# Kernel optimization log

Measured on AMD Instinct MI355X. Metric: run time of the kernel, lower is better.

The kernel has to match this reference:

```python
import jax, jax.numpy as jnp
import numpy as np

B, S, H, E = 32, 4096, 512, 512

def setup_inputs() -> dict:
    key = jax.random.key(0)
    ks = jax.random.split(key, 11)
    sc = 1.0 / np.sqrt(H)
    return {
        "context": jax.random.normal(ks[0], (B, S, H), jnp.float32),
        "h": jax.random.normal(ks[1], (B, H), jnp.float32),
        "x": jax.random.normal(ks[2], (B, E), jnp.float32),
        "We": jax.random.normal(ks[3], (H, H), jnp.float32) * sc,
        "be": jax.random.normal(ks[4], (H,), jnp.float32) * sc,
        "Wd": jax.random.normal(ks[5], (H, H), jnp.float32) * sc,
        "bd": jax.random.normal(ks[6], (H,), jnp.float32) * sc,
        "Wv": jax.random.normal(ks[7], (H,), jnp.float32) * sc,
        "bv": jax.random.normal(ks[8], (1,), jnp.float32) * sc,
        "Wr": jax.random.normal(ks[9], (2 * H, 2 * H + E), jnp.float32) * (1.0 / np.sqrt(2 * H + E)),
        "br": jax.random.normal(ks[10], (2 * H,), jnp.float32) * sc,
    }

def reference(context, h, x, We, be, Wd, bd, Wv, bv, Wr, br):
    # gamma_encoder: [B,S,H]; gamma_decoder: [B,1,H]
    ge = jnp.einsum('bsh,kh->bsk', context, We) + be
    gd = h @ Wd.T + bd
    # additive scores -> [B,S]
    scores = jnp.einsum('bsh,h->bs', jnp.tanh(ge + gd[:, None, :]), Wv) + bv[0]
    weights = jax.nn.softmax(scores, axis=1)
    # context vector c_t: [B,H]
    c_t = jnp.einsum('bs,bsh->bh', weights, context)
    # linear_r on [c_t, h, x] -> [B,2H]
    r_t = jnp.concatenate([c_t, h, x], axis=1) @ Wr.T + br
    # maxout over pairs: view [B,H,2].max(-1)
    output = jnp.max(r_t.reshape(-1, r_t.shape[1] // 2, 2), axis=2)
    return (output, weights)
```

## Files before the change

### kernel.cpp

```cpp
#include <hip/hip_runtime.h>

typedef __attribute__((ext_vector_type(8))) short bf16x8;
typedef __attribute__((ext_vector_type(16))) float f32x16;

typedef __attribute__((address_space(3))) unsigned int lds_u32;
typedef __attribute__((address_space(1))) unsigned int glb_u32;

union frag_u { bf16x8 v; unsigned int u[4]; };

__device__ inline unsigned int cvt_pk_bf16(float lo, float hi){
  unsigned int r;
  asm("v_cvt_pk_bf16_f32 %0, %1, %2" : "=v"(r) : "v"(lo), "v"(hi));
  return r;
}
__device__ inline bf16x8 pack8(float4 a, float4 b){
  union { unsigned int u[4]; bf16x8 v; } r;
  r.u[0]=cvt_pk_bf16(a.x,a.y); r.u[1]=cvt_pk_bf16(a.z,a.w);
  r.u[2]=cvt_pk_bf16(b.x,b.y); r.u[3]=cvt_pk_bf16(b.z,b.w);
  return r.v;
}
__device__ inline float fast_tanh(float x){
  float e = __builtin_amdgcn_exp2f(x * 2.8853900817779268f);
  return 1.0f - 2.0f * __builtin_amdgcn_rcpf(e + 1.0f);
}
#define PIN8(F) asm volatile("" : "+v"((F).u[0]), "+v"((F).u[1]), \
                                  "+v"((F).u[2]), "+v"((F).u[3]))
#define LOG2E 1.4426950408889634f

__global__ __launch_bounds__(256) void we_conv(const float* __restrict__ We,
                                               uint4* __restrict__ weFrag){
  int gid = blockIdx.x * 256 + threadIdx.x;
  int l  = gid & 63;
  int nc = gid >> 11;
  int t  = (gid >> 6) & 31;
  int colv = nc*32 + (l & 31);
  int k = t*16 + (l >> 5)*8;
  const float4* src = (const float4*)(We + colv*512 + k);
  float4 f0 = src[0], f1 = src[1];
  weFrag[gid] = make_uint4(cvt_pk_bf16(f0.x,f0.y), cvt_pk_bf16(f0.z,f0.w),
                           cvt_pk_bf16(f1.x,f1.y), cvt_pk_bf16(f1.z,f1.w));
}

__global__ __launch_bounds__(256) void gd_kernel(const float* __restrict__ hvec,
                                                 const float* __restrict__ Wd,
                                                 const float* __restrict__ bd,
                                                 const float* __restrict__ be,
                                                 float* __restrict__ gd){
  __shared__ float hs[512];
  int b = blockIdx.x >> 2, kc = blockIdx.x & 3;
  int tid = threadIdx.x;
  hs[tid]       = hvec[b*512 + tid];
  hs[tid + 256] = hvec[b*512 + 256 + tid];
  __syncthreads();
  int k  = kc*128 + (tid >> 1);
  int hh = (tid & 1) * 256;
  const float4* wrow = (const float4*)(Wd + (size_t)k*512 + hh);
  const float4* hv4  = (const float4*)(hs + hh);
  float acc = 0.f;
  #pragma unroll 8
  for (int i = 0; i < 64; ++i){
    float4 w = wrow[i]; float4 u = hv4[i];
    acc += w.x*u.x + w.y*u.y + w.z*u.z + w.w*u.w;
  }
  acc += __shfl_xor(acc, 1);
  if ((tid & 1) == 0) gd[b*512 + k] = acc + bd[k] + be[k];
}

__global__ __launch_bounds__(256, 2) void score_kernel(
    const float* __restrict__ ctx, const uint4* __restrict__ weFrag,
    const float* __restrict__ gd, const float* __restrict__ Wv,
    float* __restrict__ scores, float* __restrict__ ctp,
    float* __restrict__ MS){
  __shared__ char lds[2*32768 + 4096];
  __shared__ float sc_lds[128];
  __shared__ float w_lds[128];
  __shared__ float red2[2];
  char* ldsB = lds;
  float* gdwv = (float*)(lds + 65536);

  const int tid  = threadIdx.x;
  const int wid  = tid >> 6;
  const int lane = tid & 63;
  const int bid  = blockIdx.x;
  const int row0 = bid * 128;
  const int b    = bid >> 5;
  const int col  = lane & 31;
  const int hi   = lane >> 5;
  const int st   = bid & 15;

  #define ISSUE(NC, BUF) do { \
    const char* _g = (const char*)weFrag + (size_t)(NC)*32768 + wid*8192 + lane*16; \
    char* _l = ldsB + (BUF)*32768 + wid*8192; \
    _Pragma("unroll") \
    for (int _i = 0; _i < 8; ++_i) \
      __builtin_amdgcn_global_load_lds((const glb_u32*)(_g + _i*1024), \
                                       (lds_u32*)(_l + _i*1024), 16, 0, 0); \
  } while(0)

  ISSUE(st, 0);

  if (tid < 128) ((float4*)gdwv)[tid] = ((const float4*)(gd + b*512))[tid];
  else           ((float4*)gdwv)[tid] = ((const float4*)Wv)[tid - 128];

  frag_u afrag[32];
  {
    const float4* ap = (const float4*)(ctx + (size_t)(row0 + wid*32 + col)*512 + hi*8);
    #pragma unroll
    for (int t = 0; t < 32; ++t){
      afrag[t].v = pack8(ap[t*4], ap[t*4 + 1]);
      PIN8(afrag[t]);
    }
  }

  asm volatile("s_waitcnt lgkmcnt(0)" ::: "memory");

  float sc[16];
  #pragma unroll
  for (int r = 0; r < 16; ++r) sc[r] = 0.f;

  for (int nc = 0; nc < 16; ++nc){
    const int cur = (st + nc) & 15;
    asm volatile("s_waitcnt vmcnt(0)" ::: "memory");
    __builtin_amdgcn_s_barrier();
    if (nc < 15) ISSUE((cur + 1) & 15, (nc + 1) & 1);

    const char* bb = ldsB + (nc & 1)*32768 + lane*16;
    f32x16 accLo, accHi;
    #pragma unroll
    for (int r = 0; r < 16; ++r){ accLo[r] = 0.f; accHi[r] = 0.f; }

    frag_u c0, c1, c2, c3, n0, n1, n2, n3;
    c0.v = *(const bf16x8*)(bb +  0*1024);
    c1.v = *(const bf16x8*)(bb +  8*1024);
    c2.v = *(const bf16x8*)(bb + 16*1024);
    c3.v = *(const bf16x8*)(bb + 24*1024);
    PIN8(c0); PIN8(c1); PIN8(c2); PIN8(c3);

    #pragma unroll
    for (int g = 0; g < 8; ++g){
      if (g < 7){
        n0.v = *(const bf16x8*)(bb + (g + 1     )*1024);
        n1.v = *(const bf16x8*)(bb + (g + 1 +  8)*1024);
        n2.v = *(const bf16x8*)(bb + (g + 1 + 16)*1024);
        n3.v = *(const bf16x8*)(bb + (g + 1 + 24)*1024);
      }
      __builtin_amdgcn_s_setprio(1);
      accLo = __builtin_amdgcn_mfma_f32_32x32x16_bf16(afrag[g     ].v, c0.v, accLo, 0, 0, 0);
      accHi = __builtin_amdgcn_mfma_f32_32x32x16_bf16(afrag[g + 16].v, c2.v, accHi, 0, 0, 0);
      accLo = __builtin_amdgcn_mfma_f32_32x32x16_bf16(afrag[g +  8].v, c1.v, accLo, 0, 0, 0);
      accHi = __builtin_amdgcn_mfma_f32_32x32x16_bf16(afrag[g + 24].v, c3.v, accHi, 0, 0, 0);
      __builtin_amdgcn_s_setprio(0);
      if (g < 7){
        PIN8(n0); PIN8(n1); PIN8(n2); PIN8(n3);
        c0 = n0; c1 = n1; c2 = n2; c3 = n3;
      }
    }

    float gdv = gdwv[cur*32 + col];
    float wvv = gdwv[512 + cur*32 + col];
    #pragma unroll
    for (int r = 0; r < 16; ++r)
      sc[r] += fast_tanh(accLo[r] + accHi[r] + gdv) * wvv;
  }
  #undef ISSUE

  #pragma unroll
  for (int r = 0; r < 16; ++r){
    #pragma unroll
    for (int m = 1; m <= 16; m <<= 1) sc[r] += __shfl_xor(sc[r], m);
  }
  if (col == 0){
    float* so = scores + row0 + wid*32 + 4*hi;
    #pragma unroll
    for (int r = 0; r < 16; ++r){
      int rr = (r & 3) + 8*(r >> 2);
      so[rr] = sc[r];
      sc_lds[wid*32 + 4*hi + rr] = sc[r];
    }
  }
  __syncthreads();

  float M = -1e30f;
  {
    const float4* s4 = (const float4*)sc_lds;
    #pragma unroll
    for (int i = 0; i < 32; ++i){
      float4 v = s4[i];
      M = fmaxf(M, fmaxf(fmaxf(v.x, v.y), fmaxf(v.z, v.w)));
    }
  }
  if (tid < 128){
    float w = __builtin_amdgcn_exp2f((sc_lds[tid] - M) * LOG2E);
    w_lds[tid] = w;
    #pragma unroll
    for (int o = 1; o < 64; o <<= 1) w += __shfl_xor(w, o);
    if ((tid & 63) == 0) red2[tid >> 6] = w;
  }
  __syncthreads();
  float S_blk = red2[0] + red2[1];

  float ctpA = 0.f, ctpB = 0.f;
  #pragma unroll
  for (int p = 0; p < 2; ++p){
    if ((wid >> 1) == p){
      int rl = (wid & 1)*32 + col;
      char* dst = ldsB + rl*1024;
      int swz = (rl & 7) << 4;
      #pragma unroll
      for (int t = 0; t < 32; ++t)
        *(uint4*)(dst + ((t*32 + hi*16) ^ swz)) = *(uint4*)&afrag[t].u[0];
    }
    __syncthreads();
    const float* wp = w_lds + p*64;
    #pragma unroll 8
    for (int r = 0; r < 64; ++r){
      unsigned int u = *(const unsigned int*)(ldsB + r*1024 + ((tid*4) ^ ((r & 7) << 4)));
      float cw = wp[r];
      union { unsigned int q; float f; } flo, fhi;
      flo.q = u << 16;
      fhi.q = u & 0xffff0000u;
      ctpA += cw * flo.f;
      ctpB += cw * fhi.f;
    }
    __syncthreads();
  }
  ((float2*)(ctp + (size_t)bid*512))[tid] = make_float2(ctpA, ctpB);
  if (tid == 0){ MS[2*bid] = M; MS[2*bid + 1] = S_blk; }
}

__global__ __launch_bounds__(256) void combine_kernel(const float* __restrict__ ctp,
                                                      const float* __restrict__ MS,
                                                      float* __restrict__ ct,
                                                      float* __restrict__ mbuf){
  __shared__ float wsh[32];
  __shared__ float msh[2];
  int b = blockIdx.x, tid = threadIdx.x;
  if (tid < 64){
    int i = tid & 31;
    float Mi = MS[(b*32 + i)*2];
    float Si = MS[(b*32 + i)*2 + 1];
    float M = Mi;
    #pragma unroll
    for (int o = 1; o < 32; o <<= 1) M = fmaxf(M, __shfl_xor(M, o));
    float w = __builtin_amdgcn_exp2f((Mi - M) * LOG2E);
    float d = w * Si;
    #pragma unroll
    for (int o = 1; o < 32; o <<= 1) d += __shfl_xor(d, o);
    if (tid < 32) wsh[i] = w;
    if (tid == 0){ msh[0] = M; msh[1] = 1.0f / d; }
  }
  __syncthreads();
  float invd = msh[1];
  float a0 = 0.f, a1 = 0.f;
  #pragma unroll
  for (int i = 0; i < 32; ++i){
    float2 v = ((const float2*)(ctp + (size_t)(b*32 + i)*512))[tid];
    float w = wsh[i];
    a0 += w * v.x; a1 += w * v.y;
  }
  ((float2*)(ct + b*512))[tid] = make_float2(a0 * invd, a1 * invd);
  if (tid == 0){ mbuf[2*b] = msh[0]; mbuf[2*b + 1] = invd; }
}

__global__ __launch_bounds__(256) void weights_kernel(const float* __restrict__ scores,
                                                      const float* __restrict__ mbuf,
                                                      float* __restrict__ weights){
  int b = blockIdx.x, tid = threadIdx.x;
  float M = mbuf[2*b], invd = mbuf[2*b + 1];
  const float4* src = (const float4*)(scores + b*4096);
  float4* dst = (float4*)(weights + b*4096);
  #pragma unroll
  for (int i = 0; i < 4; ++i){
    float4 v = src[tid + i*256];
    v.x = __builtin_amdgcn_exp2f((v.x - M) * LOG2E) * invd;
    v.y = __builtin_amdgcn_exp2f((v.y - M) * LOG2E) * invd;
    v.z = __builtin_amdgcn_exp2f((v.z - M) * LOG2E) * invd;
    v.w = __builtin_amdgcn_exp2f((v.w - M) * LOG2E) * invd;
    dst[tid + i*256] = v;
  }
}

__global__ __launch_bounds__(256) void final_kernel(
    const float* __restrict__ ct, const float* __restrict__ hvec,
    const float* __restrict__ x, const float* __restrict__ Wr,
    const float* __restrict__ br, float* __restrict__ out){
  __shared__ float xs[8][1536];
  int bt = blockIdx.x >> 4;
  int it = blockIdx.x & 15;
  int tid = threadIdx.x;
  int b0 = bt * 8;
  for (int idx = tid; idx < 8*1536; idx += 256){
    int bl = idx / 1536, j = idx % 1536;
    int b = b0 + bl;
    float v = (j < 512) ? ct[b*512 + j]
            : (j < 1024) ? hvec[b*512 + (j - 512)]
            : x[b*512 + (j - 1024)];
    xs[bl][j] = v;
  }
  __syncthreads();
  int i = it*64 + (tid & 63);
  int bl0 = (tid >> 6) * 2;
  const float4* wrow = (const float4*)(Wr + (size_t)i*1536);
  const float4* x0 = (const float4*)xs[bl0];
  const float4* x1 = (const float4*)xs[bl0 + 1];
  float a0 = 0.f, a1 = 0.f;
  #pragma unroll 4
  for (int k = 0; k < 384; ++k){
    float4 w = wrow[k];
    float4 u0 = x0[k], u1 = x1[k];
    a0 += w.x*u0.x + w.y*u0.y + w.z*u0.z + w.w*u0.w;
    a1 += w.x*u1.x + w.y*u1.y + w.z*u1.z + w.w*u1.w;
  }
  float bias = br[i];
  a0 += bias; a1 += bias;
  float n0 = __shfl_xor(a0, 1);
  float n1 = __shfl_xor(a1, 1);
  if ((tid & 1) == 0){
    out[(b0 + bl0    )*512 + (i >> 1)] = fmaxf(a0, n0);
    out[(b0 + bl0 + 1)*512 + (i >> 1)] = fmaxf(a1, n1);
  }
}

extern "C" void kernel_launch(void* const* d_in, const int* in_sizes, int n_in,
                              void* d_out, int out_size, void* d_ws, size_t ws_size,
                              hipStream_t stream){
  const float* ctx  = (const float*)d_in[0];
  const float* hvec = (const float*)d_in[1];
  const float* x    = (const float*)d_in[2];
  const float* We   = (const float*)d_in[3];
  const float* be   = (const float*)d_in[4];
  const float* Wd   = (const float*)d_in[5];
  const float* bd   = (const float*)d_in[6];
  const float* Wv   = (const float*)d_in[7];
  const float* Wr   = (const float*)d_in[9];
  const float* br   = (const float*)d_in[10];

  float* out     = (float*)d_out;
  float* weights = out + 32*512;

  char* ws = (char*)d_ws;
  char* weFrag   = ws;
  float* scores  = (float*)(ws + (512 << 10));
  float* ctp     = (float*)(ws + (1024 << 10));
  float* MS      = (float*)(ws + (3 << 20));
  float* mbuf    = (float*)(ws + (3 << 20) + (16 << 10));
  float* ct      = (float*)(ws + (3 << 20) + (32 << 10));
  float* gd      = (float*)(ws + (3 << 20) + (96 << 10));

  we_conv<<<128, 256, 0, stream>>>(We, (uint4*)weFrag);
  gd_kernel<<<128, 256, 0, stream>>>(hvec, Wd, bd, be, gd);
  score_kernel<<<1024, 256, 0, stream>>>(ctx, (const uint4*)weFrag, gd, Wv,
                                         scores, ctp, MS);
  combine_kernel<<<32, 256, 0, stream>>>(ctp, MS, ct, mbuf);
  weights_kernel<<<32, 256, 0, stream>>>(scores, mbuf, weights);
  final_kernel<<<64, 256, 0, stream>>>(ct, hvec, x, Wr, br, out);
}
```

Baseline: 200.2 us.

## Use 512-thread score blocks sharing each We tile across 8 waves

The score kernel now runs 512 threads (8 waves) per block covering 256 context rows, so each We tile staged in LDS is reused by twice as many waves, halving total weight traffic into LDS. The weight-tile load is split into two halves, each with its own wait and barrier, so the second half's load overlaps the first half's MFMAs. The softmax partials, the context-vector reduction (one bf16 column per thread) and combine_kernel are adjusted for 16 blocks per batch. Extra barriers and 512-thread blocks may reduce scheduling flexibility, and register pressure under launch_bounds(512,4) could cause spills.

```diff
diff --git a/kernel.cpp b/kernel.cpp
--- a/kernel.cpp
+++ b/kernel.cpp
@@ -66,41 +66,69 @@
   if ((tid & 1) == 0) gd[b*512 + k] = acc + bd[k] + be[k];
 }
 
-__global__ __launch_bounds__(256, 2) void score_kernel(
+__global__ __launch_bounds__(512, 4) void score_kernel(
     const float* __restrict__ ctx, const uint4* __restrict__ weFrag,
     const float* __restrict__ gd, const float* __restrict__ Wv,
     float* __restrict__ scores, float* __restrict__ ctp,
     float* __restrict__ MS){
-  __shared__ char lds[2*32768 + 4096];
-  __shared__ float sc_lds[128];
-  __shared__ float w_lds[128];
-  __shared__ float red2[2];
-  char* ldsB = lds;
-  float* gdwv = (float*)(lds + 65536);
+  __shared__ char ldsB[2*32768];
+  __shared__ float gdwv[1024];
+  __shared__ float sc_lds[256];
+  __shared__ float w_lds[256];
+  __shared__ float red4[4];
 
   const int tid  = threadIdx.x;
   const int wid  = tid >> 6;
   const int lane = tid & 63;
   const int bid  = blockIdx.x;
-  const int row0 = bid * 128;
-  const int b    = bid >> 5;
+  const int row0 = bid * 256;
+  const int b    = bid >> 4;
   const int col  = lane & 31;
   const int hi   = lane >> 5;
   const int st   = bid & 15;
 
-  #define ISSUE(NC, BUF) do { \
-    const char* _g = (const char*)weFrag + (size_t)(NC)*32768 + wid*8192 + lane*16; \
-    char* _l = ldsB + (BUF)*32768 + wid*8192; \
+  #define ISSUE_H(NC, BUF, TR) do { \
+    int _t = (TR)*16 + wid*2; \
+    const char* _g = (const char*)weFrag + (size_t)(NC)*32768 + _t*1024 + lane*16; \
+    char* _l = ldsB + (BUF)*32768 + _t*1024; \
+    __builtin_amdgcn_global_load_lds((const glb_u32*)_g, (lds_u32*)_l, 16, 0, 0); \
+    __builtin_amdgcn_global_load_lds((const glb_u32*)(_g + 1024), \
+                                     (lds_u32*)(_l + 1024), 16, 0, 0); \
+  } while(0)
+
+  #define HALF(H) do { \
+    frag_u c0, c1, c2, c3, n0, n1, n2, n3; \
+    c0.v = *(const bf16x8*)(bb + ((H)*16 +  0)*1024); \
+    c1.v = *(const bf16x8*)(bb + ((H)*16 +  4)*1024); \
+    c2.v = *(const bf16x8*)(bb + ((H)*16 +  8)*1024); \
+    c3.v = *(const bf16x8*)(bb + ((H)*16 + 12)*1024); \
+    PIN8(c0); PIN8(c1); PIN8(c2); PIN8(c3); \
     _Pragma("unroll") \
-    for (int _i = 0; _i < 8; ++_i) \
-      __builtin_amdgcn_global_load_lds((const glb_u32*)(_g + _i*1024), \
-                                       (lds_u32*)(_l + _i*1024), 16, 0, 0); \
+    for (int g = 0; g < 4; ++g){ \
+      if (g < 3){ \
+        n0.v = *(const bf16x8*)(bb + ((H)*16 + g +  1)*1024); \
+        n1.v = *(const bf16x8*)(bb + ((H)*16 + g +  5)*1024); \
+        n2.v = *(const bf16x8*)(bb + ((H)*16 + g +  9)*1024); \
+        n3.v = *(const bf16x8*)(bb + ((H)*16 + g + 13)*1024); \
+      } \
+      __builtin_amdgcn_s_setprio(1); \
+      accLo = __builtin_amdgcn_mfma_f32_32x32x16_bf16(afrag[(H)*16 + g     ].v, c0.v, accLo, 0, 0, 0); \
+      accHi = __builtin_amdgcn_mfma_f32_32x32x16_bf16(afrag[(H)*16 + g +  4].v, c1.v, accHi, 0, 0, 0); \
+      accLo = __builtin_amdgcn_mfma_f32_32x32x16_bf16(afrag[(H)*16 + g +  8].v, c2.v, accLo, 0, 0, 0); \
+      accHi = __builtin_amdgcn_mfma_f32_32x32x16_bf16(afrag[(H)*16 + g + 12].v, c3.v, accHi, 0, 0, 0); \
+      __builtin_amdgcn_s_setprio(0); \
+      if (g < 3){ \
+        PIN8(n0); PIN8(n1); PIN8(n2); PIN8(n3); \
+        c0 = n0; c1 = n1; c2 = n2; c3 = n3; \
+      } \
+    } \
   } while(0)
 
-  ISSUE(st, 0);
-
-  if (tid < 128) ((float4*)gdwv)[tid] = ((const float4*)(gd + b*512))[tid];
-  else           ((float4*)gdwv)[tid] = ((const float4*)Wv)[tid - 128];
+  ISSUE_H(st, 0, 0);
+  ISSUE_H(st, 0, 1);
+
+  if (tid < 128)      ((float4*)gdwv)[tid] = ((const float4*)(gd + b*512))[tid];
+  else if (tid < 256) ((float4*)gdwv)[tid] = ((const float4*)Wv)[tid - 128];
 
   frag_u afrag[32];
   {
@@ -120,41 +148,26 @@
 
   for (int nc = 0; nc < 16; ++nc){
     const int cur = (st + nc) & 15;
-    asm volatile("s_waitcnt vmcnt(0)" ::: "memory");
+
+    asm volatile("s_waitcnt vmcnt(2)" ::: "memory");
     __builtin_amdgcn_s_barrier();
-    if (nc < 15) ISSUE((cur + 1) & 15, (nc + 1) & 1);
+    asm volatile("" ::: "memory");
+    if (nc < 15) ISSUE_H((st + nc + 1) & 15, (nc + 1) & 1, 0);
 
     const char* bb = ldsB + (nc & 1)*32768 + lane*16;
     f32x16 accLo, accHi;
     #pragma unroll
     for (int r = 0; r < 16; ++r){ accLo[r] = 0.f; accHi[r] = 0.f; }
 
-    frag_u c0, c1, c2, c3, n0, n1, n2, n3;
-    c0.v = *(const bf16x8*)(bb +  0*1024);
-    c1.v = *(const bf16x8*)(bb +  8*1024);
-    c2.v = *(const bf16x8*)(bb + 16*1024);
-    c3.v = *(const bf16x8*)(bb + 24*1024);
-    PIN8(c0); PIN8(c1); PIN8(c2); PIN8(c3);
-
-    #pragma unroll
-    for (int g = 0; g < 8; ++g){
-      if (g < 7){
-        n0.v = *(const bf16x8*)(bb + (g + 1     )*1024);
-        n1.v = *(const bf16x8*)(bb + (g + 1 +  8)*1024);
-        n2.v = *(const bf16x8*)(bb + (g + 1 + 16)*1024);
-        n3.v = *(const bf16x8*)(bb + (g + 1 + 24)*1024);
-      }
-      __builtin_amdgcn_s_setprio(1);
-      accLo = __builtin_amdgcn_mfma_f32_32x32x16_bf16(afrag[g     ].v, c0.v, accLo, 0, 0, 0);
-      accHi = __builtin_amdgcn_mfma_f32_32x32x16_bf16(afrag[g + 16].v, c2.v, accHi, 0, 0, 0);
-      accLo = __builtin_amdgcn_mfma_f32_32x32x16_bf16(afrag[g +  8].v, c1.v, accLo, 0, 0, 0);
-      accHi = __builtin_amdgcn_mfma_f32_32x32x16_bf16(afrag[g + 24].v, c3.v, accHi, 0, 0, 0);
-      __builtin_amdgcn_s_setprio(0);
-      if (g < 7){
-        PIN8(n0); PIN8(n1); PIN8(n2); PIN8(n3);
-        c0 = n0; c1 = n1; c2 = n2; c3 = n3;
-      }
-    }
+    HALF(0);
+
+    if (nc < 15) asm volatile("s_waitcnt vmcnt(2)" ::: "memory");
+    else         asm volatile("s_waitcnt vmcnt(0)" ::: "memory");
+    __builtin_amdgcn_s_barrier();
+    asm volatile("" ::: "memory");
+    if (nc < 15) ISSUE_H((st + nc + 1) & 15, (nc + 1) & 1, 1);
+
+    HALF(1);
 
     float gdv = gdwv[cur*32 + col];
     float wvv = gdwv[512 + cur*32 + col];
@@ -162,7 +175,8 @@
     for (int r = 0; r < 16; ++r)
       sc[r] += fast_tanh(accLo[r] + accHi[r] + gdv) * wvv;
   }
-  #undef ISSUE
+  #undef ISSUE_H
+  #undef HALF
 
   #pragma unroll
   for (int r = 0; r < 16; ++r){
@@ -184,24 +198,24 @@
   {
     const float4* s4 = (const float4*)sc_lds;
     #pragma unroll
-    for (int i = 0; i < 32; ++i){
+    for (int i = 0; i < 64; ++i){
       float4 v = s4[i];
       M = fmaxf(M, fmaxf(fmaxf(v.x, v.y), fmaxf(v.z, v.w)));
     }
   }
-  if (tid < 128){
+  if (tid < 256){
     float w = __builtin_amdgcn_exp2f((sc_lds[tid] - M) * LOG2E);
     w_lds[tid] = w;
     #pragma unroll
     for (int o = 1; o < 64; o <<= 1) w += __shfl_xor(w, o);
-    if ((tid & 63) == 0) red2[tid >> 6] = w;
-  }
-  __syncthreads();
-  float S_blk = red2[0] + red2[1];
-
-  float ctpA = 0.f, ctpB = 0.f;
-  #pragma unroll
-  for (int p = 0; p < 2; ++p){
+    if ((tid & 63) == 0) red4[tid >> 6] = w;
+  }
+  __syncthreads();
+  float S_blk = red4[0] + red4[1] + red4[2] + red4[3];
+
+  float ctp1 = 0.f;
+  #pragma unroll
+  for (int p = 0; p < 4; ++p){
     if ((wid >> 1) == p){
       int rl = (wid & 1)*32 + col;
       char* dst = ldsB + rl*1024;
@@ -214,17 +228,13 @@
     const float* wp = w_lds + p*64;
     #pragma unroll 8
     for (int r = 0; r < 64; ++r){
-      unsigned int u = *(const unsigned int*)(ldsB + r*1024 + ((tid*4) ^ ((r & 7) << 4)));
-      float cw = wp[r];
-      union { unsigned int q; float f; } flo, fhi;
-      flo.q = u << 16;
-      fhi.q = u & 0xffff0000u;
-      ctpA += cw * flo.f;
-      ctpB += cw * fhi.f;
+      unsigned int u = *(const unsigned short*)(ldsB + r*1024 + ((tid*2) ^ ((r & 7) << 4)));
+      union { unsigned int q; float f; } fv; fv.q = u << 16;
+      ctp1 += wp[r] * fv.f;
     }
     __syncthreads();
   }
-  ((float2*)(ctp + (size_t)bid*512))[tid] = make_float2(ctpA, ctpB);
+  ctp[(size_t)bid*512 + tid] = ctp1;
   if (tid == 0){ MS[2*bid] = M; MS[2*bid + 1] = S_blk; }
 }
 
@@ -232,29 +242,28 @@
                                                       const float* __restrict__ MS,
                                                       float* __restrict__ ct,
                                                       float* __restrict__ mbuf){
-  __shared__ float wsh[32];
+  __shared__ float wsh[16];
   __shared__ float msh[2];
   int b = blockIdx.x, tid = threadIdx.x;
-  if (tid < 64){
-    int i = tid & 31;
-    float Mi = MS[(b*32 + i)*2];
-    float Si = MS[(b*32 + i)*2 + 1];
+  if (tid < 16){
+    float Mi = MS[(b*16 + tid)*2];
+    float Si = MS[(b*16 + tid)*2 + 1];
     float M = Mi;
     #pragma unroll
-    for (int o = 1; o < 32; o <<= 1) M = fmaxf(M, __shfl_xor(M, o));
+    for (int o = 1; o < 16; o <<= 1) M = fmaxf(M, __shfl_xor(M, o));
     float w = __builtin_amdgcn_exp2f((Mi - M) * LOG2E);
     float d = w * Si;
     #pragma unroll
-    for (int o = 1; o < 32; o <<= 1) d += __shfl_xor(d, o);
-    if (tid < 32) wsh[i] = w;
+    for (int o = 1; o < 16; o <<= 1) d += __shfl_xor(d, o);
+    wsh[tid] = w;
     if (tid == 0){ msh[0] = M; msh[1] = 1.0f / d; }
   }
   __syncthreads();
   float invd = msh[1];
   float a0 = 0.f, a1 = 0.f;
   #pragma unroll
-  for (int i = 0; i < 32; ++i){
-    float2 v = ((const float2*)(ctp + (size_t)(b*32 + i)*512))[tid];
+  for (int i = 0; i < 16; ++i){
+    float2 v = ((const float2*)(ctp + (size_t)(b*16 + i)*512))[tid];
     float w = wsh[i];
     a0 += w * v.x; a1 += w * v.y;
   }
@@ -349,8 +358,8 @@
 
   we_conv<<<128, 256, 0, stream>>>(We, (uint4*)weFrag);
   gd_kernel<<<128, 256, 0, stream>>>(hvec, Wd, bd, be, gd);
-  score_kernel<<<1024, 256, 0, stream>>>(ctx, (const uint4*)weFrag, gd, Wv,
-                                         scores, ctp, MS);
+  score_kernel<<<512, 512, 0, stream>>>(ctx, (const uint4*)weFrag, gd, Wv,
+                                        scores, ctp, MS);
   combine_kernel<<<32, 256, 0, stream>>>(ctp, MS, ct, mbuf);
   weights_kernel<<<32, 256, 0, stream>>>(scores, mbuf, weights);
   final_kernel<<<64, 256, 0, stream>>>(ct, hvec, x, Wr, br, out);
```

After: 420.8 us. 2.1x slower.

## Widen score blocks to eight waves with a deeper shared We pipeline

Applied to the files above, without the earlier changes.

Score blocks grow from 4 to 8 waves (512 threads). Each block now processes two 256-row slabs one after the other, and all eight waves share each staged We chunk, which roughly halves the We reload traffic per row. The We staging moves from a double buffer to a 4-buffer ring with three chunks in flight, using graded vmcnt waits. The grid shrinks to 256 blocks, so combine_kernel now merges 16 partials per batch. The trade-off is about 128KB of LDS per block, which likely allows only one block per CU. The slab loop is also serialized, with context fragment loading and the softmax/context-vector epilogue no longer overlapped across blocks.

```diff
diff --git a/kernel.cpp b/kernel.cpp
--- a/kernel.cpp
+++ b/kernel.cpp
@@ -66,195 +66,199 @@
   if ((tid & 1) == 0) gd[b*512 + k] = acc + bd[k] + be[k];
 }
 
-__global__ __launch_bounds__(256, 2) void score_kernel(
+__global__ __launch_bounds__(512, 2) void score_kernel(
     const float* __restrict__ ctx, const uint4* __restrict__ weFrag,
     const float* __restrict__ gd, const float* __restrict__ Wv,
     float* __restrict__ scores, float* __restrict__ ctp,
     float* __restrict__ MS){
-  __shared__ char lds[2*32768 + 4096];
-  __shared__ float sc_lds[128];
-  __shared__ float w_lds[128];
-  __shared__ float red2[2];
-  char* ldsB = lds;
-  float* gdwv = (float*)(lds + 65536);
+  __shared__ char ldsB[4*32768];
+  __shared__ float gdwv[1024];
+  __shared__ float sc_lds[256];
+  __shared__ float w_lds[256];
+  __shared__ float red4[4];
 
   const int tid  = threadIdx.x;
   const int wid  = tid >> 6;
   const int lane = tid & 63;
   const int bid  = blockIdx.x;
-  const int row0 = bid * 128;
-  const int b    = bid >> 5;
+  const int row0 = bid * 512;
+  const int b    = bid >> 3;
   const int col  = lane & 31;
   const int hi   = lane >> 5;
   const int st   = bid & 15;
 
   #define ISSUE(NC, BUF) do { \
-    const char* _g = (const char*)weFrag + (size_t)(NC)*32768 + wid*8192 + lane*16; \
-    char* _l = ldsB + (BUF)*32768 + wid*8192; \
+    const char* _g = (const char*)weFrag + (size_t)(NC)*32768 + (wid*4)*1024 + lane*16; \
+    char* _l = ldsB + (BUF)*32768 + (wid*4)*1024; \
     _Pragma("unroll") \
-    for (int _i = 0; _i < 8; ++_i) \
+    for (int _i = 0; _i < 4; ++_i) \
       __builtin_amdgcn_global_load_lds((const glb_u32*)(_g + _i*1024), \
                                        (lds_u32*)(_l + _i*1024), 16, 0, 0); \
   } while(0)
 
-  ISSUE(st, 0);
-
-  if (tid < 128) ((float4*)gdwv)[tid] = ((const float4*)(gd + b*512))[tid];
-  else           ((float4*)gdwv)[tid] = ((const float4*)Wv)[tid - 128];
-
-  frag_u afrag[32];
-  {
-    const float4* ap = (const float4*)(ctx + (size_t)(row0 + wid*32 + col)*512 + hi*8);
-    #pragma unroll
-    for (int t = 0; t < 32; ++t){
-      afrag[t].v = pack8(ap[t*4], ap[t*4 + 1]);
-      PIN8(afrag[t]);
-    }
-  }
-
-  asm volatile("s_waitcnt lgkmcnt(0)" ::: "memory");
-
-  float sc[16];
-  #pragma unroll
-  for (int r = 0; r < 16; ++r) sc[r] = 0.f;
-
-  for (int nc = 0; nc < 16; ++nc){
-    const int cur = (st + nc) & 15;
-    asm volatile("s_waitcnt vmcnt(0)" ::: "memory");
-    __builtin_amdgcn_s_barrier();
-    if (nc < 15) ISSUE((cur + 1) & 15, (nc + 1) & 1);
-
-    const char* bb = ldsB + (nc & 1)*32768 + lane*16;
-    f32x16 accLo, accHi;
-    #pragma unroll
-    for (int r = 0; r < 16; ++r){ accLo[r] = 0.f; accHi[r] = 0.f; }
-
-    frag_u c0, c1, c2, c3, n0, n1, n2, n3;
-    c0.v = *(const bf16x8*)(bb +  0*1024);
-    c1.v = *(const bf16x8*)(bb +  8*1024);
-    c2.v = *(const bf16x8*)(bb + 16*1024);
-    c3.v = *(const bf16x8*)(bb + 24*1024);
-    PIN8(c0); PIN8(c1); PIN8(c2); PIN8(c3);
-
-    #pragma unroll
-    for (int g = 0; g < 8; ++g){
-      if (g < 7){
-        n0.v = *(const bf16x8*)(bb + (g + 1     )*1024);
-        n1.v = *(const bf16x8*)(bb + (g + 1 +  8)*1024);
-        n2.v = *(const bf16x8*)(bb + (g + 1 + 16)*1024);
-        n3.v = *(const bf16x8*)(bb + (g + 1 + 24)*1024);
-      }
-      __builtin_amdgcn_s_setprio(1);
-      accLo = __builtin_amdgcn_mfma_f32_32x32x16_bf16(afrag[g     ].v, c0.v, accLo, 0, 0, 0);
-      accHi = __builtin_amdgcn_mfma_f32_32x32x16_bf16(afrag[g + 16].v, c2.v, accHi, 0, 0, 0);
-      accLo = __builtin_amdgcn_mfma_f32_32x32x16_bf16(afrag[g +  8].v, c1.v, accLo, 0, 0, 0);
-      accHi = __builtin_amdgcn_mfma_f32_32x32x16_bf16(afrag[g + 24].v, c3.v, accHi, 0, 0, 0);
-      __builtin_amdgcn_s_setprio(0);
-      if (g < 7){
-        PIN8(n0); PIN8(n1); PIN8(n2); PIN8(n3);
-        c0 = n0; c1 = n1; c2 = n2; c3 = n3;
-      }
-    }
-
-    float gdv = gdwv[cur*32 + col];
-    float wvv = gdwv[512 + cur*32 + col];
-    #pragma unroll
-    for (int r = 0; r < 16; ++r)
-      sc[r] += fast_tanh(accLo[r] + accHi[r] + gdv) * wvv;
+  if (tid < 128)      ((float4*)gdwv)[tid] = ((const float4*)(gd + b*512))[tid];
+  else if (tid < 256) ((float4*)gdwv)[tid] = ((const float4*)Wv)[tid - 128];
+
+  for (int slab = 0; slab < 2; ++slab){
+    const int srow = row0 + slab*256;
+
+    frag_u afrag[32];
+    {
+      const float4* ap = (const float4*)(ctx + (size_t)(srow + wid*32 + col)*512 + hi*8);
+      #pragma unroll
+      for (int t = 0; t < 32; ++t){
+        afrag[t].v = pack8(ap[t*4], ap[t*4 + 1]);
+        PIN8(afrag[t]);
+      }
+    }
+    asm volatile("s_waitcnt lgkmcnt(0)" ::: "memory");
+
+    ISSUE(st, 0);
+    ISSUE((st + 1) & 15, 1);
+    ISSUE((st + 2) & 15, 2);
+
+    float sc[16];
+    #pragma unroll
+    for (int r = 0; r < 16; ++r) sc[r] = 0.f;
+
+    for (int nc = 0; nc < 16; ++nc){
+      const int cur = (st + nc) & 15;
+
+      if (nc <= 13)      asm volatile("s_waitcnt vmcnt(8)" ::: "memory");
+      else if (nc == 14) asm volatile("s_waitcnt vmcnt(4)" ::: "memory");
+      else               asm volatile("s_waitcnt vmcnt(0)" ::: "memory");
+      __builtin_amdgcn_s_barrier();
+      if (nc < 13) ISSUE((st + nc + 3) & 15, (nc + 3) & 3);
+
+      const char* bb = ldsB + (nc & 3)*32768 + lane*16;
+      f32x16 accLo, accHi;
+      #pragma unroll
+      for (int r = 0; r < 16; ++r){ accLo[r] = 0.f; accHi[r] = 0.f; }
+
+      frag_u c0, c1, c2, c3, n0, n1, n2, n3;
+      c0.v = *(const bf16x8*)(bb +  0*1024);
+      c1.v = *(const bf16x8*)(bb +  8*1024);
+      c2.v = *(const bf16x8*)(bb + 16*1024);
+      c3.v = *(const bf16x8*)(bb + 24*1024);
+      PIN8(c0); PIN8(c1); PIN8(c2); PIN8(c3);
+
+      #pragma unroll
+      for (int g = 0; g < 8; ++g){
+        if (g < 7){
+          n0.v = *(const bf16x8*)(bb + (g + 1     )*1024);
+          n1.v = *(const bf16x8*)(bb + (g + 1 +  8)*1024);
+          n2.v = *(const bf16x8*)(bb + (g + 1 + 16)*1024);
+          n3.v = *(const bf16x8*)(bb + (g + 1 + 24)*1024);
+        }
+        __builtin_amdgcn_s_setprio(1);
+        accLo = __builtin_amdgcn_mfma_f32_32x32x16_bf16(afrag[g     ].v, c0.v, accLo, 0, 0, 0);
+        accHi = __builtin_amdgcn_mfma_f32_32x32x16_bf16(afrag[g + 16].v, c2.v, accHi, 0, 0, 0);
+        accLo = __builtin_amdgcn_mfma_f32_32x32x16_bf16(afrag[g +  8].v, c1.v, accLo, 0, 0, 0);
+        accHi = __builtin_amdgcn_mfma_f32_32x32x16_bf16(afrag[g + 24].v, c3.v, accHi, 0, 0, 0);
+        __builtin_amdgcn_s_setprio(0);
+        if (g < 7){
+          PIN8(n0); PIN8(n1); PIN8(n2); PIN8(n3);
+          c0 = n0; c1 = n1; c2 = n2; c3 = n3;
+        }
+      }
+
+      float gdv = gdwv[cur*32 + col];
+      float wvv = gdwv[512 + cur*32 + col];
+      #pragma unroll
+      for (int r = 0; r < 16; ++r)
+        sc[r] += fast_tanh(accLo[r] + accHi[r] + gdv) * wvv;
+    }
+
+    #pragma unroll
+    for (int r = 0; r < 16; ++r){
+      #pragma unroll
+      for (int m = 1; m <= 16; m <<= 1) sc[r] += __shfl_xor(sc[r], m);
+    }
+    if (col == 0){
+      float* so = scores + srow + wid*32 + 4*hi;
+      #pragma unroll
+      for (int r = 0; r < 16; ++r){
+        int rr = (r & 3) + 8*(r >> 2);
+        so[rr] = sc[r];
+        sc_lds[wid*32 + 4*hi + rr] = sc[r];
+      }
+    }
+    __syncthreads();
+
+    float M = -1e30f;
+    {
+      const float4* s4 = (const float4*)sc_lds;
+      #pragma unroll
+      for (int i = 0; i < 64; ++i){
+        float4 v = s4[i];
+        M = fmaxf(M, fmaxf(fmaxf(v.x, v.y), fmaxf(v.z, v.w)));
+      }
+    }
+    if (tid < 256){
+      float w = __builtin_amdgcn_exp2f((sc_lds[tid] - M) * LOG2E);
+      w_lds[tid] = w;
+      #pragma unroll
+      for (int o = 1; o < 64; o <<= 1) w += __shfl_xor(w, o);
+      if ((tid & 63) == 0) red4[tid >> 6] = w;
+    }
+    __syncthreads();
+    float S_blk = red4[0] + red4[1] + red4[2] + red4[3];
+
+    float ctp1 = 0.f;
+    #pragma unroll
+    for (int p = 0; p < 4; ++p){
+      if ((wid >> 1) == p){
+        int rl = (wid & 1)*32 + col;
+        char* dst = ldsB + rl*1024;
+        int swz = (rl & 7) << 4;
+        #pragma unroll
+        for (int t = 0; t < 32; ++t)
+          *(uint4*)(dst + ((t*32 + hi*16) ^ swz)) = *(uint4*)&afrag[t].u[0];
+      }
+      __syncthreads();
+      const float* wp = w_lds + p*64;
+      #pragma unroll 8
+      for (int r = 0; r < 64; ++r){
+        unsigned int u = *(const unsigned short*)(ldsB + r*1024 + ((tid*2) ^ ((r & 7) << 4)));
+        union { unsigned int q; float f; } fv; fv.q = u << 16;
+        ctp1 += wp[r] * fv.f;
+      }
+      __syncthreads();
+    }
+    const int sid = bid*2 + slab;
+    ctp[(size_t)sid*512 + tid] = ctp1;
+    if (tid == 0){ MS[2*sid] = M; MS[2*sid + 1] = S_blk; }
+    __syncthreads();
   }
   #undef ISSUE
-
-  #pragma unroll
-  for (int r = 0; r < 16; ++r){
-    #pragma unroll
-    for (int m = 1; m <= 16; m <<= 1) sc[r] += __shfl_xor(sc[r], m);
-  }
-  if (col == 0){
-    float* so = scores + row0 + wid*32 + 4*hi;
-    #pragma unroll
-    for (int r = 0; r < 16; ++r){
-      int rr = (r & 3) + 8*(r >> 2);
-      so[rr] = sc[r];
-      sc_lds[wid*32 + 4*hi + rr] = sc[r];
-    }
-  }
-  __syncthreads();
-
-  float M = -1e30f;
-  {
-    const float4* s4 = (const float4*)sc_lds;
-    #pragma unroll
-    for (int i = 0; i < 32; ++i){
-      float4 v = s4[i];
-      M = fmaxf(M, fmaxf(fmaxf(v.x, v.y), fmaxf(v.z, v.w)));
-    }
-  }
-  if (tid < 128){
-    float w = __builtin_amdgcn_exp2f((sc_lds[tid] - M) * LOG2E);
-    w_lds[tid] = w;
-    #pragma unroll
-    for (int o = 1; o < 64; o <<= 1) w += __shfl_xor(w, o);
-    if ((tid & 63) == 0) red2[tid >> 6] = w;
-  }
-  __syncthreads();
-  float S_blk = red2[0] + red2[1];
-
-  float ctpA = 0.f, ctpB = 0.f;
-  #pragma unroll
-  for (int p = 0; p < 2; ++p){
-    if ((wid >> 1) == p){
-      int rl = (wid & 1)*32 + col;
-      char* dst = ldsB + rl*1024;
-      int swz = (rl & 7) << 4;
-      #pragma unroll
-      for (int t = 0; t < 32; ++t)
-        *(uint4*)(dst + ((t*32 + hi*16) ^ swz)) = *(uint4*)&afrag[t].u[0];
-    }
-    __syncthreads();
-    const float* wp = w_lds + p*64;
-    #pragma unroll 8
-    for (int r = 0; r < 64; ++r){
-      unsigned int u = *(const unsigned int*)(ldsB + r*1024 + ((tid*4) ^ ((r & 7) << 4)));
-      float cw = wp[r];
-      union { unsigned int q; float f; } flo, fhi;
-      flo.q = u << 16;
-      fhi.q = u & 0xffff0000u;
-      ctpA += cw * flo.f;
-      ctpB += cw * fhi.f;
-    }
-    __syncthreads();
-  }
-  ((float2*)(ctp + (size_t)bid*512))[tid] = make_float2(ctpA, ctpB);
-  if (tid == 0){ MS[2*bid] = M; MS[2*bid + 1] = S_blk; }
 }
 
 __global__ __launch_bounds__(256) void combine_kernel(const float* __restrict__ ctp,
                                                       const float* __restrict__ MS,
                                                       float* __restrict__ ct,
                                                       float* __restrict__ mbuf){
-  __shared__ float wsh[32];
+  __shared__ float wsh[16];
   __shared__ float msh[2];
   int b = blockIdx.x, tid = threadIdx.x;
-  if (tid < 64){
-    int i = tid & 31;
-    float Mi = MS[(b*32 + i)*2];
-    float Si = MS[(b*32 + i)*2 + 1];
+  if (tid < 16){
+    float Mi = MS[(b*16 + tid)*2];
+    float Si = MS[(b*16 + tid)*2 + 1];
     float M = Mi;
     #pragma unroll
-    for (int o = 1; o < 32; o <<= 1) M = fmaxf(M, __shfl_xor(M, o));
+    for (int o = 1; o < 16; o <<= 1) M = fmaxf(M, __shfl_xor(M, o));
     float w = __builtin_amdgcn_exp2f((Mi - M) * LOG2E);
     float d = w * Si;
     #pragma unroll
-    for (int o = 1; o < 32; o <<= 1) d += __shfl_xor(d, o);
-    if (tid < 32) wsh[i] = w;
+    for (int o = 1; o < 16; o <<= 1) d += __shfl_xor(d, o);
+    wsh[tid] = w;
     if (tid == 0){ msh[0] = M; msh[1] = 1.0f / d; }
   }
   __syncthreads();
   float invd = msh[1];
   float a0 = 0.f, a1 = 0.f;
   #pragma unroll
-  for (int i = 0; i < 32; ++i){
-    float2 v = ((const float2*)(ctp + (size_t)(b*32 + i)*512))[tid];
+  for (int i = 0; i < 16; ++i){
+    float2 v = ((const float2*)(ctp + (size_t)(b*16 + i)*512))[tid];
     float w = wsh[i];
     a0 += w * v.x; a1 += w * v.y;
   }
@@ -349,8 +353,8 @@
 
   we_conv<<<128, 256, 0, stream>>>(We, (uint4*)weFrag);
   gd_kernel<<<128, 256, 0, stream>>>(hvec, Wd, bd, be, gd);
-  score_kernel<<<1024, 256, 0, stream>>>(ctx, (const uint4*)weFrag, gd, Wv,
-                                         scores, ctp, MS);
+  score_kernel<<<256, 512, 0, stream>>>(ctx, (const uint4*)weFrag, gd, Wv,
+                                        scores, ctp, MS);
   combine_kernel<<<32, 256, 0, stream>>>(ctp, MS, ct, mbuf);
   weights_kernel<<<32, 256, 0, stream>>>(scores, mbuf, weights);
   final_kernel<<<64, 256, 0, stream>>>(ct, hvec, x, Wr, br, out);
```

Result: slower. 222.0 us (+10.8%).
